# Performance work log

Hardware: AMD Instinct MI355X
Metric: run time of the kernel (lower is better)

## Reference

```python
import jax, jax.numpy as jnp
import numpy as np

HEADS = 8
DIM_HEAD = 64
QUERY_DIM = 512
CONTEXT_DIM = 768
INNER = HEADS * DIM_HEAD  # 512
SCALE = DIM_HEAD ** -0.5


def setup_inputs() -> dict:
    key = jax.random.key(0)
    ks = jax.random.split(key, 7)
    B, N, M = 4, 2048, 2048
    x = jax.random.normal(ks[0], (B, N, QUERY_DIM), dtype=jnp.float32)
    context = jax.random.normal(ks[1], (B, M, CONTEXT_DIM), dtype=jnp.float32)
    # torch Linear weights: [out_features, in_features], y = x @ W.T
    s = 0.02
    Wq = jax.random.normal(ks[2], (INNER, QUERY_DIM), dtype=jnp.float32) * s
    Wk = jax.random.normal(ks[3], (INNER, CONTEXT_DIM), dtype=jnp.float32) * s
    Wv = jax.random.normal(ks[4], (INNER, CONTEXT_DIM), dtype=jnp.float32) * s
    Wo = jax.random.normal(ks[5], (QUERY_DIM, INNER), dtype=jnp.float32) * s
    bo = jax.random.normal(ks[6], (QUERY_DIM,), dtype=jnp.float32) * s
    return {"x": x, "context": context, "Wq": Wq, "Wk": Wk, "Wv": Wv, "Wo": Wo, "bo": bo}


def reference(x, context, Wq, Wk, Wv, Wo, bo):
    b, n, _ = x.shape
    m = context.shape[1]
    h, d = HEADS, DIM_HEAD
    # Projections (bias=False for q/k/v)
    q = jnp.einsum('bnc,ec->bne', x, Wq)        # [b, n, inner]
    k = jnp.einsum('bmc,ec->bme', context, Wk)  # [b, m, inner]
    v = jnp.einsum('bmc,ec->bme', context, Wv)
    # Split heads
    q = q.reshape(b, n, h, d)
    k = k.reshape(b, m, h, d)
    v = v.reshape(b, m, h, d)
    # Scores in fp32 (original casts q,k to float), scaled by dim_head**-0.5
    sim = jnp.einsum('bihd,bjhd->bhij', q.astype(jnp.float32), k.astype(jnp.float32)) * SCALE
    attn = jax.nn.softmax(sim, axis=-1).astype(v.dtype)
    out = jnp.einsum('bhij,bjhd->bihd', attn, v).reshape(b, n, h * d)
    # Output projection with bias (dropout=0 -> identity)
    return jnp.einsum('bne,oe->bno', out, Wo) + bo
```

## Files before the change

### kernel.cpp

```cpp
#include <hip/hip_runtime.h>
#include <hip/hip_bf16.h>
#include <math.h>


typedef __bf16 bf16x8 __attribute__((ext_vector_type(8)));
typedef __bf16 bf16x4 __attribute__((ext_vector_type(4)));
typedef short s16x4 __attribute__((ext_vector_type(4)));
typedef float f32x4 __attribute__((ext_vector_type(4)));

#define QSCALE 0.18033688011112042f

#if __has_builtin(__builtin_amdgcn_exp2f)
#define EXP2(x) __builtin_amdgcn_exp2f(x)
#else
#define EXP2(x) exp2f(x)
#endif

__device__ __forceinline__ f32x4 mfma32(bf16x8 a, bf16x8 b, f32x4 c) {
  return __builtin_amdgcn_mfma_f32_16x16x32_bf16(a, b, c, 0, 0, 0);
}
__device__ __forceinline__ f32x4 mfma16(s16x4 a, s16x4 b, f32x4 c) {
  return __builtin_amdgcn_mfma_f32_16x16x16bf16_1k(a, b, c, 0, 0, 0);
}

__global__ __launch_bounds__(256) void cast_all(
    const float* __restrict__ x, const float* __restrict__ ctx,
    const float* __restrict__ wq, const float* __restrict__ wk,
    const float* __restrict__ wv, const float* __restrict__ wo,
    __bf16* __restrict__ xb, __bf16* __restrict__ cb,
    __bf16* __restrict__ wqb, __bf16* __restrict__ wkb,
    __bf16* __restrict__ wvb, __bf16* __restrict__ wob) {
  const int B0 = 1048576;
  const int B1 = 2621440;
  const int B2 = 2686976;
  const int B3 = 2785280;
  const int B4 = 2883584;
  const int B5 = 2949120;
  for (int i = blockIdx.x * blockDim.x + threadIdx.x; i < B5;
       i += gridDim.x * blockDim.x) {
    const float* s;
    __bf16* d;
    int off;
    if (i < B0)      { s = x;   d = xb;  off = i; }
    else if (i < B1) { s = ctx; d = cb;  off = i - B0; }
    else if (i < B2) { s = wq;  d = wqb; off = i - B1; }
    else if (i < B3) { s = wk;  d = wkb; off = i - B2; }
    else if (i < B4) { s = wv;  d = wvb; off = i - B3; }
    else             { s = wo;  d = wob; off = i - B4; }
    float4 f = ((const float4*)s)[off];
    union { __bf16 b[4]; ushort4 u; } cv;
    cv.b[0] = (__bf16)f.x; cv.b[1] = (__bf16)f.y;
    cv.b[2] = (__bf16)f.z; cv.b[3] = (__bf16)f.w;
    ((ushort4*)d)[off] = cv.u;
  }
}

template <int MODE>
__device__ __forceinline__ void gemm_body64(
    const __bf16* __restrict__ A, const __bf16* __restrict__ B,
    __bf16* __restrict__ Cout, int Kd, float scale, int m0, int n0,
    __bf16 (*As)[40], __bf16 (*Bs)[40]) {
  const int t = threadIdx.x;
  const int w = t >> 6;
  const int lane = t & 63;
  const int ln = lane & 15;
  const int qd = lane >> 4;
  const int wm = (w >> 1) * 32;
  const int wn = (w & 1) * 64;

  f32x4 zero4 = {0.f, 0.f, 0.f, 0.f};
  f32x4 acc[2][4];
#pragma unroll
  for (int i = 0; i < 2; ++i)
#pragma unroll
    for (int j = 0; j < 4; ++j) acc[i][j] = zero4;

  const int ra = t >> 2, ca = (t & 3) * 8;
  const int rb = t >> 1, cbx = (t & 1) * 16;
  const __bf16* gA = A + (size_t)(m0 + ra) * Kd + ca;
  const __bf16* gB = B + (size_t)(n0 + rb) * Kd + cbx;

  for (int kc = 0; kc < Kd; kc += 32) {
    uint4 a0 = *(const uint4*)(gA + kc);
    uint4 b0 = *(const uint4*)(gB + kc);
    uint4 b1 = *(const uint4*)(gB + kc + 8);
    __syncthreads();
    *(uint4*)&As[ra][ca] = a0;
    *(uint4*)&Bs[rb][cbx] = b0;
    *(uint4*)&Bs[rb][cbx + 8] = b1;
    __syncthreads();
    bf16x8 af[2], bfr[4];
#pragma unroll
    for (int i = 0; i < 2; ++i)
      af[i] = *(const bf16x8*)&As[wm + i * 16 + ln][qd * 8];
#pragma unroll
    for (int j = 0; j < 4; ++j)
      bfr[j] = *(const bf16x8*)&Bs[wn + j * 16 + ln][qd * 8];
#pragma unroll
    for (int i = 0; i < 2; ++i)
#pragma unroll
      for (int j = 0; j < 4; ++j) {
        if (MODE == 1)
          acc[i][j] = mfma32(af[i], bfr[j], acc[i][j]);
        else
          acc[i][j] = mfma32(bfr[j], af[i], acc[i][j]);
      }
  }

#pragma unroll
  for (int i = 0; i < 2; ++i)
#pragma unroll
    for (int j = 0; j < 4; ++j) {
      if (MODE == 0) {
        const int gm = m0 + wm + i * 16 + ln;
        const int gn0 = n0 + wn + j * 16 + qd * 4;
        const int bb = gm >> 11, tok = gm & 2047;
        const int hh = gn0 >> 6, dd0 = gn0 & 63;
        bf16x4 v;
#pragma unroll
        for (int rg = 0; rg < 4; ++rg) v[rg] = (__bf16)(acc[i][j][rg] * scale);
        *(bf16x4*)(Cout + (((size_t)bb * 8 + hh) * 2048 + tok) * 64 + dd0) = v;
      } else {
        const int gm0 = m0 + wm + i * 16 + qd * 4;
        const int gn = n0 + wn + j * 16 + ln;
        const int bb = gm0 >> 11, tok0 = gm0 & 2047;
        const int hh = gn >> 6, dd = gn & 63;
        bf16x4 v;
#pragma unroll
        for (int rg = 0; rg < 4; ++rg) v[rg] = (__bf16)acc[i][j][rg];
        *(bf16x4*)(Cout + (((size_t)bb * 8 + hh) * 64 + dd) * 2048 + tok0) = v;
      }
    }
}

__global__ __launch_bounds__(256, 4) void proj_qkv(
    const __bf16* __restrict__ xb, const __bf16* __restrict__ cb,
    const __bf16* __restrict__ Wq, const __bf16* __restrict__ Wk,
    const __bf16* __restrict__ Wv, __bf16* __restrict__ Qw,
    __bf16* __restrict__ Kw, __bf16* __restrict__ Vtw) {
  __shared__ __bf16 As[64][40];
  __shared__ __bf16 Bs[128][40];
  const int m0 = blockIdx.x * 64;
  const int job = blockIdx.y >> 2;
  const int n0 = (blockIdx.y & 3) * 128;
  if (job == 0)
    gemm_body64<0>(xb, Wq, Qw, 512, QSCALE, m0, n0, As, Bs);
  else if (job == 1)
    gemm_body64<0>(cb, Wk, Kw, 768, 1.0f, m0, n0, As, Bs);
  else
    gemm_body64<1>(cb, Wv, Vtw, 768, 1.0f, m0, n0, As, Bs);
}

__global__ __launch_bounds__(256, 4) void gemm_out(
    const __bf16* __restrict__ O0, const __bf16* __restrict__ O1,
    const float* __restrict__ lbuf,
    const __bf16* __restrict__ B,
    float* __restrict__ C, const float* __restrict__ bias) {
  const int m0 = blockIdx.x * 64;
  const int n0 = blockIdx.y * 64;
  const int t = threadIdx.x;
  const int w = t >> 6;
  const int lane = t & 63;
  const int ln = lane & 15;
  const int qd = lane >> 4;
  const int wm = (w >> 1) * 32;
  const int wn = (w & 1) * 32;

  __shared__ __bf16 As[64][40];
  __shared__ __bf16 Bs[64][40];

  f32x4 zero4 = {0.f, 0.f, 0.f, 0.f};
  f32x4 acc[2][2];
#pragma unroll
  for (int i = 0; i < 2; ++i)
#pragma unroll
    for (int j = 0; j < 2; ++j) acc[i][j] = zero4;

  const int ra = t >> 2, ca = (t & 3) * 8;
  const int gm_s = m0 + ra;
  const int bidx = gm_s >> 11, tok_s = gm_s & 2047;
  const size_t aoff = (size_t)gm_s * 512 + ca;
  const __bf16* gB = B + (size_t)(n0 + ra) * 512 + ca;

  float inv[8];
#pragma unroll
  for (int hh = 0; hh < 8; ++hh) {
    const float l0 = lbuf[((size_t)bidx * 8 + hh) * 2048 + tok_s];
    const float l1 = lbuf[65536 + ((size_t)bidx * 8 + hh) * 2048 + tok_s];
    inv[hh] = 1.0f / (l0 + l1);
  }

  for (int kc = 0; kc < 512; kc += 32) {
    const float iv = inv[kc >> 6];
    union { bf16x8 v; uint4 u; } u0, u1, rr;
    u0.u = *(const uint4*)(O0 + aoff + kc);
    u1.u = *(const uint4*)(O1 + aoff + kc);
    uint4 bv = *(const uint4*)(gB + kc);
#pragma unroll
    for (int e = 0; e < 8; ++e)
      rr.v[e] = (__bf16)(((float)u0.v[e] + (float)u1.v[e]) * iv);
    __syncthreads();
    *(uint4*)&As[ra][ca] = rr.u;
    *(uint4*)&Bs[ra][ca] = bv;
    __syncthreads();
    bf16x8 af[2], bfr[2];
#pragma unroll
    for (int i = 0; i < 2; ++i)
      af[i] = *(const bf16x8*)&As[wm + i * 16 + ln][qd * 8];
#pragma unroll
    for (int j = 0; j < 2; ++j)
      bfr[j] = *(const bf16x8*)&Bs[wn + j * 16 + ln][qd * 8];
#pragma unroll
    for (int i = 0; i < 2; ++i)
#pragma unroll
      for (int j = 0; j < 2; ++j)
        acc[i][j] = mfma32(bfr[j], af[i], acc[i][j]);
  }

#pragma unroll
  for (int i = 0; i < 2; ++i)
#pragma unroll
    for (int j = 0; j < 2; ++j) {
      const int gm = m0 + wm + i * 16 + ln;
      const int gn0 = n0 + wn + j * 16 + qd * 4;
      f32x4 bi = *(const f32x4*)&bias[gn0];
      f32x4 v = acc[i][j] + bi;
      *(f32x4*)&C[(size_t)gm * 512 + gn0] = v;
    }
}

__global__ __launch_bounds__(256, 4) void attn_kernel(
    const __bf16* __restrict__ Q,
    const __bf16* __restrict__ K,
    const __bf16* __restrict__ Vt,
    __bf16* __restrict__ Oh,
    float* __restrict__ lbuf) {
  const int S = 2048;
  const int qt = blockIdx.x;
  const int bh = blockIdx.y;
  const int sp = blockIdx.z;
  const int b = bh >> 3, h = bh & 7;
  const int t = threadIdx.x;
  const int w = t >> 6;
  const int lane = t & 63;
  const int ln = lane & 15;
  const int qd = lane >> 4;

  __shared__ __align__(16) __bf16 Ks[128][72];
  __shared__ __align__(16) __bf16 Vts[64][132];

  bf16x8 bq[2][2];
  {
    const __bf16* qb =
        Q + ((size_t)bh * S + qt * 128 + w * 32 + ln) * 64 + qd * 8;
#pragma unroll
    for (int mt = 0; mt < 2; ++mt)
#pragma unroll
      for (int kst = 0; kst < 2; ++kst)
        bq[mt][kst] = *(const bf16x8*)(qb + mt * 1024 + kst * 32);
  }

  f32x4 zero4 = {0.f, 0.f, 0.f, 0.f};
  f32x4 o[2][4];
  f32x4 o_l[2];
#pragma unroll
  for (int mt = 0; mt < 2; ++mt) {
#pragma unroll
    for (int i = 0; i < 4; ++i) o[mt][i] = zero4;
    o_l[mt] = zero4;
  }
  const s16x4 ones = {0x3F80, 0x3F80, 0x3F80, 0x3F80};

  const int kr = t >> 1, kc = (t & 1) * 32;
  const int vd = t >> 2, vc = (t & 3) * 32;
  const int kt0 = sp * 8;

  for (int kt = kt0; kt < kt0 + 8; ++kt) {
    const uint4* gK =
        (const uint4*)(K + ((size_t)bh * S + kt * 128 + kr) * 64 + kc);
    const uint4* gV =
        (const uint4*)(Vt + ((size_t)bh * 64 + vd) * S + kt * 128 + vc);
    uint4 kv0 = gK[0], kv1 = gK[1], kv2 = gK[2], kv3 = gK[3];
    uint4 vv0 = gV[0], vv1 = gV[1], vv2 = gV[2], vv3 = gV[3];
    __syncthreads();
    {
      uint4* dK = (uint4*)&Ks[kr][kc];
      dK[0] = kv0; dK[1] = kv1; dK[2] = kv2; dK[3] = kv3;
      uint2* dV = (uint2*)&Vts[vd][vc];
      dV[0] = *(uint2*)&vv0; dV[1] = *((uint2*)&vv0 + 1);
      dV[2] = *(uint2*)&vv1; dV[3] = *((uint2*)&vv1 + 1);
      dV[4] = *(uint2*)&vv2; dV[5] = *((uint2*)&vv2 + 1);
      dV[6] = *(uint2*)&vv3; dV[7] = *((uint2*)&vv3 + 1);
    }
    __syncthreads();

#pragma unroll
    for (int c = 0; c < 4; ++c) {
      f32x4 s[2][2];
      s[0][0] = zero4; s[0][1] = zero4; s[1][0] = zero4; s[1][1] = zero4;
#pragma unroll
      for (int e = 0; e < 2; ++e) {
        const int nt = c * 2 + e;
#pragma unroll
        for (int kst = 0; kst < 2; ++kst) {
          bf16x8 ak = *(const bf16x8*)&Ks[nt * 16 + ln][kst * 32 + qd * 8];
          s[e][0] = mfma32(ak, bq[0][kst], s[e][0]);
          s[e][1] = mfma32(ak, bq[1][kst], s[e][1]);
        }
      }
#pragma unroll
      for (int e = 0; e < 2; ++e)
#pragma unroll
        for (int mt = 0; mt < 2; ++mt)
#pragma unroll
          for (int rg = 0; rg < 4; ++rg) s[e][mt][rg] = EXP2(s[e][mt][rg]);
#pragma unroll
      for (int e = 0; e < 2; ++e) {
        const int nt = c * 2 + e;
        bf16x4 c0, c1;
#pragma unroll
        for (int rg = 0; rg < 4; ++rg) {
          c0[rg] = (__bf16)s[e][0][rg];
          c1[rg] = (__bf16)s[e][1][rg];
        }
        s16x4 p0 = __builtin_bit_cast(s16x4, c0);
        s16x4 p1 = __builtin_bit_cast(s16x4, c1);
        o_l[0] = mfma16(ones, p0, o_l[0]);
        o_l[1] = mfma16(ones, p1, o_l[1]);
#pragma unroll
        for (int i = 0; i < 4; ++i) {
          bf16x4 av = *(const bf16x4*)&Vts[i * 16 + ln][nt * 16 + qd * 4];
          s16x4 a = __builtin_bit_cast(s16x4, av);
          o[0][i] = mfma16(a, p0, o[0][i]);
          o[1][i] = mfma16(a, p1, o[1][i]);
        }
      }
    }
  }

  __bf16* Osp = Oh + (size_t)sp * 8192 * 512;
#pragma unroll
  for (int mt = 0; mt < 2; ++mt) {
    const int tok = qt * 128 + w * 32 + mt * 16 + ln;
    if (qd == 0) lbuf[((size_t)sp * 32 + bh) * 2048 + tok] = o_l[mt][0];
#pragma unroll
    for (int i = 0; i < 4; ++i) {
      bf16x4 v;
#pragma unroll
      for (int rg = 0; rg < 4; ++rg) v[rg] = (__bf16)o[mt][i][rg];
      const int col = h * 64 + i * 16 + qd * 4;
      *(bf16x4*)&Osp[((size_t)b * S + tok) * 512 + col] = v;
    }
  }
}

extern "C" void kernel_launch(void* const* d_in, const int* in_sizes, int n_in,
                              void* d_out, int out_size, void* d_ws,
                              size_t ws_size, hipStream_t stream) {
  const float* x = (const float*)d_in[0];
  const float* ctx = (const float*)d_in[1];
  const float* Wq = (const float*)d_in[2];
  const float* Wk = (const float*)d_in[3];
  const float* Wv = (const float*)d_in[4];
  const float* Wo = (const float*)d_in[5];
  const float* bo = (const float*)d_in[6];

  char* p = (char*)d_ws;
  __bf16* xb = (__bf16*)p;   p += (size_t)8192 * 512 * 2;
  __bf16* cb = (__bf16*)p;   p += (size_t)8192 * 768 * 2;
  __bf16* wqb = (__bf16*)p;  p += (size_t)512 * 512 * 2;
  __bf16* wkb = (__bf16*)p;  p += (size_t)512 * 768 * 2;
  __bf16* wvb = (__bf16*)p;  p += (size_t)512 * 768 * 2;
  __bf16* wob = (__bf16*)p;  p += (size_t)512 * 512 * 2;
  __bf16* Qw = (__bf16*)p;   p += (size_t)8192 * 512 * 2;
  __bf16* Kw = (__bf16*)p;   p += (size_t)8192 * 512 * 2;
  __bf16* Vtw = (__bf16*)p;  p += (size_t)8192 * 512 * 2;
  __bf16* Oh = (__bf16*)p;   p += (size_t)2 * 8192 * 512 * 2;
  float* lbuf = (float*)p;   p += (size_t)2 * 32 * 2048 * 4;

  cast_all<<<2880, 256, 0, stream>>>(x, ctx, Wq, Wk, Wv, Wo, xb, cb, wqb, wkb,
                                     wvb, wob);

  dim3 gp(128, 12);
  proj_qkv<<<gp, 256, 0, stream>>>(xb, cb, wqb, wkb, wvb, Qw, Kw, Vtw);

  dim3 ga(16, 32, 2);
  attn_kernel<<<ga, 256, 0, stream>>>(Qw, Kw, Vtw, Oh, lbuf);

  dim3 go(128, 8);
  gemm_out<<<go, 256, 0, stream>>>(Oh, Oh + (size_t)8192 * 512, lbuf, wob,
                                   (float*)d_out, bo);
}
```

Measured before the change: 202.6 us.

## Use 16x16x32 MFMA for PV with permuted K rows; widen GEMM tiles

The attention PV product now uses the 16x16x32 bf16 MFMA instead of pairs of 16x16x16 ops. This is enabled by permuting K rows in shared memory and storing V in four per-chunk slabs, so each lane's 8 probabilities line up with contiguous V columns. Separately, the QKV projection tile widens to 64x256 and the output GEMM becomes 32x256 with occupancy hints lowered, reducing A-tile reloads at the cost of more registers and shared memory per block. The K row permutation must exactly match the MFMA output layout, or the results will be wrong.

```diff
diff --git a/kernel.cpp b/kernel.cpp
--- a/kernel.cpp
+++ b/kernel.cpp
@@ -5,7 +5,6 @@
 
 typedef __bf16 bf16x8 __attribute__((ext_vector_type(8)));
 typedef __bf16 bf16x4 __attribute__((ext_vector_type(4)));
-typedef short s16x4 __attribute__((ext_vector_type(4)));
 typedef float f32x4 __attribute__((ext_vector_type(4)));
 
 #define QSCALE 0.18033688011112042f
@@ -18,9 +17,6 @@
 
 __device__ __forceinline__ f32x4 mfma32(bf16x8 a, bf16x8 b, f32x4 c) {
   return __builtin_amdgcn_mfma_f32_16x16x32_bf16(a, b, c, 0, 0, 0);
-}
-__device__ __forceinline__ f32x4 mfma16(s16x4 a, s16x4 b, f32x4 c) {
-  return __builtin_amdgcn_mfma_f32_16x16x16bf16_1k(a, b, c, 0, 0, 0);
 }
 
 __global__ __launch_bounds__(256) void cast_all(
@@ -56,8 +52,8 @@
 }
 
 template <int MODE>
-__device__ __forceinline__ void gemm_body64(
-    const __bf16* __restrict__ A, const __bf16* __restrict__ B,
+__device__ __forceinline__ void proj_body(
+    const __bf16* __restrict__ A, const __bf16* __restrict__ W,
     __bf16* __restrict__ Cout, int Kd, float scale, int m0, int n0,
     __bf16 (*As)[40], __bf16 (*Bs)[40]) {
   const int t = threadIdx.x;
@@ -66,51 +62,53 @@
   const int ln = lane & 15;
   const int qd = lane >> 4;
   const int wm = (w >> 1) * 32;
-  const int wn = (w & 1) * 64;
+  const int wn = (w & 1) * 128;
 
   f32x4 zero4 = {0.f, 0.f, 0.f, 0.f};
-  f32x4 acc[2][4];
+  f32x4 acc[2][8];
 #pragma unroll
   for (int i = 0; i < 2; ++i)
 #pragma unroll
-    for (int j = 0; j < 4; ++j) acc[i][j] = zero4;
+    for (int j = 0; j < 8; ++j) acc[i][j] = zero4;
 
   const int ra = t >> 2, ca = (t & 3) * 8;
-  const int rb = t >> 1, cbx = (t & 1) * 16;
   const __bf16* gA = A + (size_t)(m0 + ra) * Kd + ca;
-  const __bf16* gB = B + (size_t)(n0 + rb) * Kd + cbx;
+  const __bf16* gB = W + (size_t)(n0 + t) * Kd;
 
   for (int kc = 0; kc < Kd; kc += 32) {
     uint4 a0 = *(const uint4*)(gA + kc);
     uint4 b0 = *(const uint4*)(gB + kc);
     uint4 b1 = *(const uint4*)(gB + kc + 8);
+    uint4 b2 = *(const uint4*)(gB + kc + 16);
+    uint4 b3 = *(const uint4*)(gB + kc + 24);
     __syncthreads();
     *(uint4*)&As[ra][ca] = a0;
-    *(uint4*)&Bs[rb][cbx] = b0;
-    *(uint4*)&Bs[rb][cbx + 8] = b1;
-    __syncthreads();
-    bf16x8 af[2], bfr[4];
+    *(uint4*)&Bs[t][0] = b0;
+    *(uint4*)&Bs[t][8] = b1;
+    *(uint4*)&Bs[t][16] = b2;
+    *(uint4*)&Bs[t][24] = b3;
+    __syncthreads();
+    bf16x8 af[2];
 #pragma unroll
     for (int i = 0; i < 2; ++i)
       af[i] = *(const bf16x8*)&As[wm + i * 16 + ln][qd * 8];
 #pragma unroll
-    for (int j = 0; j < 4; ++j)
-      bfr[j] = *(const bf16x8*)&Bs[wn + j * 16 + ln][qd * 8];
-#pragma unroll
-    for (int i = 0; i < 2; ++i)
-#pragma unroll
-      for (int j = 0; j < 4; ++j) {
+    for (int j = 0; j < 8; ++j) {
+      bf16x8 bfr = *(const bf16x8*)&Bs[wn + j * 16 + ln][qd * 8];
+#pragma unroll
+      for (int i = 0; i < 2; ++i) {
         if (MODE == 1)
-          acc[i][j] = mfma32(af[i], bfr[j], acc[i][j]);
+          acc[i][j] = mfma32(af[i], bfr, acc[i][j]);
         else
-          acc[i][j] = mfma32(bfr[j], af[i], acc[i][j]);
-      }
+          acc[i][j] = mfma32(bfr, af[i], acc[i][j]);
+      }
+    }
   }
 
 #pragma unroll
   for (int i = 0; i < 2; ++i)
 #pragma unroll
-    for (int j = 0; j < 4; ++j) {
+    for (int j = 0; j < 8; ++j) {
       if (MODE == 0) {
         const int gm = m0 + wm + i * 16 + ln;
         const int gn0 = n0 + wn + j * 16 + qd * 4;
@@ -133,54 +131,52 @@
     }
 }
 
-__global__ __launch_bounds__(256, 4) void proj_qkv(
+__global__ __launch_bounds__(256, 3) void proj_qkv(
     const __bf16* __restrict__ xb, const __bf16* __restrict__ cb,
     const __bf16* __restrict__ Wq, const __bf16* __restrict__ Wk,
     const __bf16* __restrict__ Wv, __bf16* __restrict__ Qw,
     __bf16* __restrict__ Kw, __bf16* __restrict__ Vtw) {
   __shared__ __bf16 As[64][40];
-  __shared__ __bf16 Bs[128][40];
+  __shared__ __bf16 Bs[256][40];
   const int m0 = blockIdx.x * 64;
-  const int job = blockIdx.y >> 2;
-  const int n0 = (blockIdx.y & 3) * 128;
+  const int job = blockIdx.y >> 1;
+  const int n0 = (blockIdx.y & 1) * 256;
   if (job == 0)
-    gemm_body64<0>(xb, Wq, Qw, 512, QSCALE, m0, n0, As, Bs);
+    proj_body<0>(xb, Wq, Qw, 512, QSCALE, m0, n0, As, Bs);
   else if (job == 1)
-    gemm_body64<0>(cb, Wk, Kw, 768, 1.0f, m0, n0, As, Bs);
+    proj_body<0>(cb, Wk, Kw, 768, 1.0f, m0, n0, As, Bs);
   else
-    gemm_body64<1>(cb, Wv, Vtw, 768, 1.0f, m0, n0, As, Bs);
-}
-
-__global__ __launch_bounds__(256, 4) void gemm_out(
+    proj_body<1>(cb, Wv, Vtw, 768, 1.0f, m0, n0, As, Bs);
+}
+
+__global__ __launch_bounds__(256, 3) void gemm_out(
     const __bf16* __restrict__ O0, const __bf16* __restrict__ O1,
     const float* __restrict__ lbuf,
     const __bf16* __restrict__ B,
     float* __restrict__ C, const float* __restrict__ bias) {
-  const int m0 = blockIdx.x * 64;
-  const int n0 = blockIdx.y * 64;
+  const int m0 = blockIdx.x * 32;
+  const int n0 = blockIdx.y * 256;
   const int t = threadIdx.x;
   const int w = t >> 6;
   const int lane = t & 63;
   const int ln = lane & 15;
   const int qd = lane >> 4;
-  const int wm = (w >> 1) * 32;
-  const int wn = (w & 1) * 32;
-
-  __shared__ __bf16 As[64][40];
-  __shared__ __bf16 Bs[64][40];
+  const int wm = (w >> 1) * 16;
+  const int wn = (w & 1) * 128;
+
+  __shared__ __bf16 As[32][40];
+  __shared__ __bf16 Bs[256][40];
 
   f32x4 zero4 = {0.f, 0.f, 0.f, 0.f};
-  f32x4 acc[2][2];
-#pragma unroll
-  for (int i = 0; i < 2; ++i)
-#pragma unroll
-    for (int j = 0; j < 2; ++j) acc[i][j] = zero4;
-
-  const int ra = t >> 2, ca = (t & 3) * 8;
+  f32x4 acc[8];
+#pragma unroll
+  for (int j = 0; j < 8; ++j) acc[j] = zero4;
+
+  const int ra = t >> 3, ca = (t & 7) * 4;
   const int gm_s = m0 + ra;
   const int bidx = gm_s >> 11, tok_s = gm_s & 2047;
   const size_t aoff = (size_t)gm_s * 512 + ca;
-  const __bf16* gB = B + (size_t)(n0 + ra) * 512 + ca;
+  const __bf16* gB = B + (size_t)(n0 + t) * 512;
 
   float inv[8];
 #pragma unroll
@@ -192,41 +188,39 @@
 
   for (int kc = 0; kc < 512; kc += 32) {
     const float iv = inv[kc >> 6];
-    union { bf16x8 v; uint4 u; } u0, u1, rr;
-    u0.u = *(const uint4*)(O0 + aoff + kc);
-    u1.u = *(const uint4*)(O1 + aoff + kc);
-    uint4 bv = *(const uint4*)(gB + kc);
-#pragma unroll
-    for (int e = 0; e < 8; ++e)
+    union { bf16x4 v; uint2 u; } u0, u1, rr;
+    u0.u = *(const uint2*)(O0 + aoff + kc);
+    u1.u = *(const uint2*)(O1 + aoff + kc);
+    uint4 b0 = *(const uint4*)(gB + kc);
+    uint4 b1 = *(const uint4*)(gB + kc + 8);
+    uint4 b2 = *(const uint4*)(gB + kc + 16);
+    uint4 b3 = *(const uint4*)(gB + kc + 24);
+#pragma unroll
+    for (int e = 0; e < 4; ++e)
       rr.v[e] = (__bf16)(((float)u0.v[e] + (float)u1.v[e]) * iv);
     __syncthreads();
-    *(uint4*)&As[ra][ca] = rr.u;
-    *(uint4*)&Bs[ra][ca] = bv;
-    __syncthreads();
-    bf16x8 af[2], bfr[2];
-#pragma unroll
-    for (int i = 0; i < 2; ++i)
-      af[i] = *(const bf16x8*)&As[wm + i * 16 + ln][qd * 8];
-#pragma unroll
-    for (int j = 0; j < 2; ++j)
-      bfr[j] = *(const bf16x8*)&Bs[wn + j * 16 + ln][qd * 8];
-#pragma unroll
-    for (int i = 0; i < 2; ++i)
-#pragma unroll
-      for (int j = 0; j < 2; ++j)
-        acc[i][j] = mfma32(bfr[j], af[i], acc[i][j]);
-  }
-
-#pragma unroll
-  for (int i = 0; i < 2; ++i)
-#pragma unroll
-    for (int j = 0; j < 2; ++j) {
-      const int gm = m0 + wm + i * 16 + ln;
-      const int gn0 = n0 + wn + j * 16 + qd * 4;
-      f32x4 bi = *(const f32x4*)&bias[gn0];
-      f32x4 v = acc[i][j] + bi;
-      *(f32x4*)&C[(size_t)gm * 512 + gn0] = v;
-    }
+    *(uint2*)&As[ra][ca] = rr.u;
+    *(uint4*)&Bs[t][0] = b0;
+    *(uint4*)&Bs[t][8] = b1;
+    *(uint4*)&Bs[t][16] = b2;
+    *(uint4*)&Bs[t][24] = b3;
+    __syncthreads();
+    bf16x8 af = *(const bf16x8*)&As[wm + ln][qd * 8];
+#pragma unroll
+    for (int j = 0; j < 8; ++j) {
+      bf16x8 bfr = *(const bf16x8*)&Bs[wn + j * 16 + ln][qd * 8];
+      acc[j] = mfma32(bfr, af, acc[j]);
+    }
+  }
+
+#pragma unroll
+  for (int j = 0; j < 8; ++j) {
+    const int gm = m0 + wm + ln;
+    const int gn0 = n0 + wn + j * 16 + qd * 4;
+    f32x4 bi = *(const f32x4*)&bias[gn0];
+    f32x4 v = acc[j] + bi;
+    *(f32x4*)&C[(size_t)gm * 512 + gn0] = v;
+  }
 }
 
 __global__ __launch_bounds__(256, 4) void attn_kernel(
@@ -247,7 +241,7 @@
   const int qd = lane >> 4;
 
   __shared__ __align__(16) __bf16 Ks[128][72];
-  __shared__ __align__(16) __bf16 Vts[64][132];
+  __shared__ __align__(16) __bf16 V4[4][64][40];
 
   bf16x8 bq[2][2];
   {
@@ -269,28 +263,33 @@
     for (int i = 0; i < 4; ++i) o[mt][i] = zero4;
     o_l[mt] = zero4;
   }
-  const s16x4 ones = {0x3F80, 0x3F80, 0x3F80, 0x3F80};
+  bf16x8 ones8;
+  {
+    union { unsigned short u[8]; bf16x8 v; } U;
+#pragma unroll
+    for (int e = 0; e < 8; ++e) U.u[e] = 0x3F80;
+    ones8 = U.v;
+  }
 
   const int kr = t >> 1, kc = (t & 1) * 32;
-  const int vd = t >> 2, vc = (t & 3) * 32;
+  const int krow =
+      (kr & ~31) | ((kr & 4) << 2) | (((kr >> 3) & 3) << 2) | (kr & 3);
+  const int vd = t >> 2, cV = t & 3;
   const int kt0 = sp * 8;
 
   for (int kt = kt0; kt < kt0 + 8; ++kt) {
     const uint4* gK =
         (const uint4*)(K + ((size_t)bh * S + kt * 128 + kr) * 64 + kc);
     const uint4* gV =
-        (const uint4*)(Vt + ((size_t)bh * 64 + vd) * S + kt * 128 + vc);
+        (const uint4*)(Vt + ((size_t)bh * 64 + vd) * S + kt * 128 + cV * 32);
     uint4 kv0 = gK[0], kv1 = gK[1], kv2 = gK[2], kv3 = gK[3];
     uint4 vv0 = gV[0], vv1 = gV[1], vv2 = gV[2], vv3 = gV[3];
     __syncthreads();
     {
-      uint4* dK = (uint4*)&Ks[kr][kc];
+      uint4* dK = (uint4*)&Ks[krow][kc];
       dK[0] = kv0; dK[1] = kv1; dK[2] = kv2; dK[3] = kv3;
-      uint2* dV = (uint2*)&Vts[vd][vc];
-      dV[0] = *(uint2*)&vv0; dV[1] = *((uint2*)&vv0 + 1);
-      dV[2] = *(uint2*)&vv1; dV[3] = *((uint2*)&vv1 + 1);
-      dV[4] = *(uint2*)&vv2; dV[5] = *((uint2*)&vv2 + 1);
-      dV[6] = *(uint2*)&vv3; dV[7] = *((uint2*)&vv3 + 1);
+      uint4* dV = (uint4*)&V4[cV][vd][0];
+      dV[0] = vv0; dV[1] = vv1; dV[2] = vv2; dV[3] = vv3;
     }
     __syncthreads();
 
@@ -314,26 +313,22 @@
         for (int mt = 0; mt < 2; ++mt)
 #pragma unroll
           for (int rg = 0; rg < 4; ++rg) s[e][mt][rg] = EXP2(s[e][mt][rg]);
-#pragma unroll
-      for (int e = 0; e < 2; ++e) {
-        const int nt = c * 2 + e;
-        bf16x4 c0, c1;
+      bf16x8 p[2];
+#pragma unroll
+      for (int mt = 0; mt < 2; ++mt) {
 #pragma unroll
         for (int rg = 0; rg < 4; ++rg) {
-          c0[rg] = (__bf16)s[e][0][rg];
-          c1[rg] = (__bf16)s[e][1][rg];
+          p[mt][rg] = (__bf16)s[0][mt][rg];
+          p[mt][rg + 4] = (__bf16)s[1][mt][rg];
         }
-        s16x4 p0 = __builtin_bit_cast(s16x4, c0);
-        s16x4 p1 = __builtin_bit_cast(s16x4, c1);
-        o_l[0] = mfma16(ones, p0, o_l[0]);
-        o_l[1] = mfma16(ones, p1, o_l[1]);
-#pragma unroll
-        for (int i = 0; i < 4; ++i) {
-          bf16x4 av = *(const bf16x4*)&Vts[i * 16 + ln][nt * 16 + qd * 4];
-          s16x4 a = __builtin_bit_cast(s16x4, av);
-          o[0][i] = mfma16(a, p0, o[0][i]);
-          o[1][i] = mfma16(a, p1, o[1][i]);
-        }
+      }
+      o_l[0] = mfma32(ones8, p[0], o_l[0]);
+      o_l[1] = mfma32(ones8, p[1], o_l[1]);
+#pragma unroll
+      for (int i = 0; i < 4; ++i) {
+        bf16x8 av = *(const bf16x8*)&V4[c][i * 16 + ln][qd * 8];
+        o[0][i] = mfma32(av, p[0], o[0][i]);
+        o[1][i] = mfma32(av, p[1], o[1][i]);
       }
     }
   }
@@ -381,13 +376,13 @@
   cast_all<<<2880, 256, 0, stream>>>(x, ctx, Wq, Wk, Wv, Wo, xb, cb, wqb, wkb,
                                      wvb, wob);
 
-  dim3 gp(128, 12);
+  dim3 gp(128, 6);
   proj_qkv<<<gp, 256, 0, stream>>>(xb, cb, wqb, wkb, wvb, Qw, Kw, Vtw);
 
   dim3 ga(16, 32, 2);
   attn_kernel<<<ga, 256, 0, stream>>>(Qw, Kw, Vtw, Oh, lbuf);
 
-  dim3 go(128, 8);
+  dim3 go(256, 2);
   gemm_out<<<go, 256, 0, stream>>>(Oh, Oh + (size_t)8192 * 512, lbuf, wob,
                                    (float*)d_out, bo);
 }
```

Measured after the change: 204.8 us. No clear change (+1.1%).
